# Optimization experiments

Hardware: AMD Instinct MI355X
Metric: run time of the kernel (lower is better)

The kernel has to match this reference:

```python
import jax, jax.numpy as jnp
import numpy as np

E4M3_MAX = 448.0  # max representable value of float8_e4m3fn


def _updated_scale(amax_history, amax_now, scale):
    # roll history, insert current amax, take running max (delayed scaling)
    hist = jnp.roll(amax_history, 1).at[0].set(amax_now)
    amax = jnp.max(hist)
    sf = E4M3_MAX / amax  # scale factor (margin = 0)
    sf = jnp.where((amax > 0.0) & jnp.isfinite(amax), sf, 1.0 / scale)
    return 1.0 / sf  # dequant scale


def _qdq(x, scale, amax_history):
    # quantize-dequantize through float8_e4m3fn with dynamic amax-history scaling
    amax_now = jnp.max(jnp.abs(x)).astype(jnp.float32)
    s = _updated_scale(amax_history, amax_now, scale[0])
    q = jnp.clip(x / s, -E4M3_MAX, E4M3_MAX).astype(jnp.float8_e4m3fn)
    return q.astype(x.dtype) * s


def setup_inputs() -> dict:
    key = jax.random.key(0)
    k1, k2 = jax.random.split(key, 2)
    B, S, D, F = 4, 2048, 4096, 16384
    HL = 16  # amax_history_length
    inputs = jax.random.normal(k1, (B, S, D), jnp.float32)
    # lecun_normal: std = 1/sqrt(fan_in)
    kernel = jax.random.normal(k2, (D, F), jnp.float32) * (1.0 / np.sqrt(D))
    bias = jnp.zeros((F,), jnp.float32)
    return {
        "inputs": inputs,
        "kernel": kernel,
        "bias": bias,
        "input_scale": jnp.ones((1,), jnp.float32),
        "input_amax_history": jnp.zeros((HL,), jnp.float32),
        "kernel_scale": jnp.ones((1,), jnp.float32),
        "kernel_amax_history": jnp.zeros((HL,), jnp.float32),
        "output_grad_scale": jnp.ones((1,), jnp.float32),
        "output_grad_amax_history": jnp.zeros((HL,), jnp.float32),
    }


def reference(inputs, kernel, bias, input_scale, input_amax_history,
              kernel_scale, kernel_amax_history, output_grad_scale,
              output_grad_amax_history):
    B, S, D = inputs.shape
    x = inputs.reshape(-1, D)  # (B*S, D)
    q_x = _qdq(x, input_scale, input_amax_history)
    q_k = _qdq(kernel, kernel_scale, kernel_amax_history)
    out = q_x @ q_k  # (B*S, F)
    # bias is rounded fp32->bf16->fp32 per the module
    b = bias.astype(jnp.bfloat16).astype(jnp.float32)
    out = jax.nn.gelu(out + b)
    return out.reshape(B, S, -1)
```

## Files before the change

### kernel.cpp

```cpp
#include <hip/hip_runtime.h>
#include <hip/hip_bf16.h>

typedef __attribute__((ext_vector_type(4))) int i32x4;
typedef __attribute__((ext_vector_type(8))) int i32x8;
typedef __attribute__((ext_vector_type(16))) float f32x16;

#define E4M3_MAX 448.0f
#define AS1 __attribute__((address_space(1)))
#define AS3 __attribute__((address_space(3)))

__device__ __forceinline__ float clip448(float v) {
  return fminf(fmaxf(v, -E4M3_MAX), E4M3_MAX);
}

__device__ __forceinline__ void gld_lds16(const void* g, void* l) {
  __builtin_amdgcn_global_load_lds((const AS1 void*)g, (AS3 void*)l, 16, 0, 0);
}

__device__ __forceinline__ float gelu_f(float v) {
  float y = 0.7978845608028654f * (v + 0.044715f * v * v * v);
  float a = fabsf(y);
  float z = __expf(-2.f * a);
  float th = (1.f - z) / (1.f + z);
  th = copysignf(th, y);
  return 0.5f * v * (1.f + th);
}

__global__ void init_ws_kernel(unsigned int* amax) {
  amax[0] = 0u;
  amax[1] = 0u;
}

__global__ void amax_kernel(const float* __restrict__ x, long n4,
                            unsigned int* __restrict__ amax_out) {
  long i0 = (long)blockIdx.x * blockDim.x + threadIdx.x;
  long stride = (long)gridDim.x * blockDim.x;
  const float4* x4 = (const float4*)x;
  float m = 0.f;
  for (long i = i0; i < n4; i += stride) {
    float4 v = x4[i];
    m = fmaxf(m, fmaxf(fmaxf(fabsf(v.x), fabsf(v.y)), fmaxf(fabsf(v.z), fabsf(v.w))));
  }
#pragma unroll
  for (int off = 32; off >= 1; off >>= 1)
    m = fmaxf(m, __shfl_xor(m, off));
  __shared__ float wmax[8];
  int wid = threadIdx.x >> 6;
  if ((threadIdx.x & 63) == 0) wmax[wid] = m;
  __syncthreads();
  if (threadIdx.x == 0) {
    int nw = blockDim.x >> 6;
    float bm = wmax[0];
    for (int w = 1; w < nw; ++w) bm = fmaxf(bm, wmax[w]);
    atomicMax(amax_out, __float_as_uint(bm));
  }
}

__global__ void scale_kernel(const unsigned int* __restrict__ amax,
                             const float* __restrict__ scale_x,
                             const float* __restrict__ hist_x,
                             const float* __restrict__ scale_k,
                             const float* __restrict__ hist_k,
                             int hl, float* __restrict__ scales) {
  if (threadIdx.x != 0) return;
  float ax = __uint_as_float(amax[0]);
  for (int i = 0; i < hl - 1; ++i) ax = fmaxf(ax, hist_x[i]);
  float sfx = E4M3_MAX / ax;
  if (!(ax > 0.f && isfinite(ax))) sfx = 1.f / scale_x[0];
  float sx = 1.f / sfx;
  float ak = __uint_as_float(amax[1]);
  for (int i = 0; i < hl - 1; ++i) ak = fmaxf(ak, hist_k[i]);
  float sfk = E4M3_MAX / ak;
  if (!(ak > 0.f && isfinite(ak))) sfk = 1.f / scale_k[0];
  float sk = 1.f / sfk;
  scales[0] = sx;
  scales[1] = sk;
  scales[2] = sx * sk;
}


__global__ void quant_x_kernel(const float* __restrict__ x,
                               unsigned char* __restrict__ Aq,
                               const float* __restrict__ scales, int K) {
  const float s = scales[0];
  const int kt = blockIdx.x, mt = blockIdx.y, nkt = gridDim.x;
  __shared__ float lt[128][68];
  const int t = threadIdx.x;
  const float* src = x + (size_t)mt * 128 * K + (size_t)kt * 64;
#pragma unroll
  for (int it = 0; it < 8; ++it) {
    int row = it * 16 + (t >> 4);
    int c4 = (t & 15) * 4;
    float4 v = *(const float4*)&src[(size_t)row * K + c4];
    lt[row][c4 + 0] = v.x; lt[row][c4 + 1] = v.y;
    lt[row][c4 + 2] = v.z; lt[row][c4 + 3] = v.w;
  }
  __syncthreads();
  uint4* out = (uint4*)(Aq + ((size_t)mt * nkt + kt) * 8192);
#pragma unroll
  for (int cc = 0; cc < 2; ++cc) {
    int c = t * 2 + cc;
    int g = c >> 7, h = (c >> 6) & 1, l = c & 63;
    int row = g * 32 + (l & 31);
    int kb = (l >> 5) * 32 + h * 16;
    unsigned int w[4];
#pragma unroll
    for (int q = 0; q < 4; ++q) {
      int b = kb + q * 4;
      int p = 0;
      p = __builtin_amdgcn_cvt_pk_fp8_f32(clip448(lt[row][b+0] / s), clip448(lt[row][b+1] / s), p, false);
      p = __builtin_amdgcn_cvt_pk_fp8_f32(clip448(lt[row][b+2] / s), clip448(lt[row][b+3] / s), p, true);
      w[q] = (unsigned int)p;
    }
    out[c] = make_uint4(w[0], w[1], w[2], w[3]);
  }
}

__global__ void quant_k_kernel(const float* __restrict__ w,
                               unsigned char* __restrict__ Bq,
                               const float* __restrict__ scales, int N) {
  const float s = scales[1];
  const int kt = blockIdx.x, nt = blockIdx.y, nkt = gridDim.x;
  __shared__ float lt[64][132];
  const int t = threadIdx.x;
  const float* src = w + (size_t)kt * 64 * N + (size_t)nt * 128;
#pragma unroll
  for (int it = 0; it < 8; ++it) {
    int row = it * 8 + (t >> 5);
    int c4 = (t & 31) * 4;
    float4 v = *(const float4*)&src[(size_t)row * N + c4];
    lt[row][c4 + 0] = v.x; lt[row][c4 + 1] = v.y;
    lt[row][c4 + 2] = v.z; lt[row][c4 + 3] = v.w;
  }
  __syncthreads();
  uint4* out = (uint4*)(Bq + ((size_t)nt * nkt + kt) * 8192);
#pragma unroll
  for (int cc = 0; cc < 2; ++cc) {
    int c = t * 2 + cc;
    int g = c >> 7, h = (c >> 6) & 1, l = c & 63;
    int nl = g * 32 + (l & 31);
    int kb = (l >> 5) * 32 + h * 16;
    unsigned int w4[4];
#pragma unroll
    for (int q = 0; q < 4; ++q) {
      int b = kb + q * 4;
      int p = 0;
      p = __builtin_amdgcn_cvt_pk_fp8_f32(clip448(lt[b+0][nl] / s), clip448(lt[b+1][nl] / s), p, false);
      p = __builtin_amdgcn_cvt_pk_fp8_f32(clip448(lt[b+2][nl] / s), clip448(lt[b+3][nl] / s), p, true);
      w4[q] = (unsigned int)p;
    }
    out[c] = make_uint4(w4[0], w4[1], w4[2], w4[3]);
  }
}

__global__ __launch_bounds__(512, 2) void gemm_fp8_kernel(
    const unsigned char* __restrict__ Aq, const unsigned char* __restrict__ Bq,
    const float* __restrict__ bias, const float* __restrict__ scales,
    float* __restrict__ C, int M, int N, int K) {
  __shared__ __align__(16) unsigned char lds[65536];
  const float s_xk = scales[2];
  const int nkt = K >> 6;
  const int t = threadIdx.x;
  const int lane = t & 63;
  const int wid = t >> 6;
  const int wm = wid >> 2, wn = wid & 3;

  int f = blockIdx.y * gridDim.x + blockIdx.x;
  int cpx = (gridDim.x * gridDim.y) >> 3;
  int f2 = (f & 7) * cpx + (f >> 3);
  int bx = f2 % gridDim.x;
  int by = f2 / gridDim.x;

  const size_t strideT = (size_t)nkt * 8192;
  const unsigned char* gA = Aq + (size_t)(2 * by) * strideT + t * 16;
  const unsigned char* gB = Bq + (size_t)(2 * bx) * strideT + t * 16;

  f32x16 acc[4][2];
#pragma unroll
  for (int i = 0; i < 4; ++i)
#pragma unroll
    for (int j = 0; j < 2; ++j)
#pragma unroll
      for (int r = 0; r < 16; ++r) acc[i][j][r] = 0.f;

  auto stage = [&](int buf, int kt_) {
    size_t o = (size_t)kt_ * 8192;
    unsigned char* l = lds + buf * 32768 + wid * 1024;
    gld_lds16(gA + o,           l);
    gld_lds16(gA + strideT + o, l + 8192);
    gld_lds16(gB + o,           l + 16384);
    gld_lds16(gB + strideT + o, l + 24576);
  };

  auto compute = [&](int buf) {
    const unsigned char* la = lds + buf * 32768;
    const unsigned char* lb = la + 16384;
    i32x8 av[4], bv[2];
#pragma unroll
    for (int i = 0; i < 4; ++i) {
      int g = wm * 4 + i;
      i32x4 lo = *(const i32x4*)&la[g * 2048 + lane * 16];
      i32x4 hi = *(const i32x4*)&la[g * 2048 + 1024 + lane * 16];
      av[i] = __builtin_shufflevector(lo, hi, 0, 1, 2, 3, 4, 5, 6, 7);
    }
#pragma unroll
    for (int j = 0; j < 2; ++j) {
      int g = wn * 2 + j;
      i32x4 lo = *(const i32x4*)&lb[g * 2048 + lane * 16];
      i32x4 hi = *(const i32x4*)&lb[g * 2048 + 1024 + lane * 16];
      bv[j] = __builtin_shufflevector(lo, hi, 0, 1, 2, 3, 4, 5, 6, 7);
    }
    __builtin_amdgcn_s_setprio(1);
#pragma unroll
    for (int i = 0; i < 4; ++i)
#pragma unroll
      for (int j = 0; j < 2; ++j)
        acc[i][j] = __builtin_amdgcn_mfma_scale_f32_32x32x64_f8f6f4(
            av[i], bv[j], acc[i][j], 0, 0, 0, 127, 0, 127);
    __builtin_amdgcn_s_setprio(0);
  };

  stage(0, 0);
  int buf = 0;
  for (int kt = 0; kt < nkt - 1; ++kt) {
    stage(buf ^ 1, kt + 1);
    asm volatile("s_waitcnt vmcnt(4)" ::: "memory");
    __builtin_amdgcn_s_barrier();
    asm volatile("" ::: "memory");
    compute(buf);
    asm volatile("" ::: "memory");
    __builtin_amdgcn_s_barrier();
    buf ^= 1;
  }
  asm volatile("s_waitcnt vmcnt(0)" ::: "memory");
  __builtin_amdgcn_s_barrier();
  asm volatile("" ::: "memory");
  compute(buf);

  const int m0 = by * 256;
  const int n0 = bx * 256;
  float bb[2];
#pragma unroll
  for (int j = 0; j < 2; ++j) {
    int col = n0 + wn * 64 + j * 32 + (lane & 31);
    bb[j] = __bfloat162float(__float2bfloat16(bias[col]));
  }
#pragma unroll
  for (int i = 0; i < 4; ++i) {
    int rowbase = m0 + wm * 128 + i * 32 + 4 * (lane >> 5);
#pragma unroll
    for (int j = 0; j < 2; ++j) {
      int col = n0 + wn * 64 + j * 32 + (lane & 31);
#pragma unroll
      for (int r = 0; r < 16; ++r) {
        int row = rowbase + (r & 3) + 8 * (r >> 2);
        float v = acc[i][j][r] * s_xk + bb[j];
        C[(size_t)row * N + col] = gelu_f(v);
      }
    }
  }
}

extern "C" void kernel_launch(void* const* d_in, const int* in_sizes, int n_in,
                              void* d_out, int out_size, void* d_ws, size_t ws_size,
                              hipStream_t stream) {
  const float* inputs = (const float*)d_in[0];
  const float* kernelw = (const float*)d_in[1];
  const float* bias = (const float*)d_in[2];
  const float* input_scale = (const float*)d_in[3];
  const float* input_hist = (const float*)d_in[4];
  const float* kernel_scale = (const float*)d_in[5];
  const float* kernel_hist = (const float*)d_in[6];

  const int F = in_sizes[2];
  const int D = in_sizes[1] / F;
  const long M = (long)in_sizes[0] / D;
  const int HL = in_sizes[4];
  const int N = F, K = D;

  unsigned int* amax = (unsigned int*)d_ws;
  float* scales = (float*)((char*)d_ws + 16);
  unsigned char* Aq = (unsigned char*)d_ws + 64;
  unsigned char* Bq = Aq + (size_t)M * K;

  float* C = (float*)d_out;

  init_ws_kernel<<<1, 1, 0, stream>>>(amax);
  amax_kernel<<<2048, 256, 0, stream>>>(inputs, (long)M * K / 4, &amax[0]);
  amax_kernel<<<2048, 256, 0, stream>>>(kernelw, (long)K * N / 4, &amax[1]);
  scale_kernel<<<1, 64, 0, stream>>>(amax, input_scale, input_hist, kernel_scale,
                                     kernel_hist, HL, scales);
  quant_x_kernel<<<dim3(K / 64, M / 128), 256, 0, stream>>>(inputs, Aq, scales, K);
  quant_k_kernel<<<dim3(K / 64, N / 128), 256, 0, stream>>>(kernelw, Bq, scales, N);
  gemm_fp8_kernel<<<dim3(N / 256, M / 256), 512, 0, stream>>>(Aq, Bq, bias, scales, C,
                                                              (int)M, N, K);
}
```

Before: 779.0 us.

## Shrink GEMM tile to 256x128 with register double-buffered fragments

Halves the N extent of each GEMM block tile from 256 to 128. LDS use drops to 48KB and each block now stages three 16-byte loads per k-step instead of four. The main loop is unrolled by two and prefetches the next k-step's LDS fragments into a second register set while the current MFMAs run. Output stores become nontemporal. Each block now does half the MFMAs per k-step, which lowers arithmetic intensity and doubles the grid and the total A-tile traffic, in exchange for more overlap and lower register and LDS pressure.

```diff
diff --git a/kernel.cpp b/kernel.cpp
--- a/kernel.cpp
+++ b/kernel.cpp
@@ -153,11 +153,41 @@
   }
 }
 
+#define BUFSZ 24576
+
+#define RD_FRAGS(av, bv, bufbase)                                              \
+  {                                                                            \
+    const unsigned char* la_ = lds + (bufbase);                                \
+    _Pragma("unroll") for (int i_ = 0; i_ < 4; ++i_) {                         \
+      int g_ = wm * 4 + i_;                                                    \
+      const unsigned char* p_ =                                                \
+          la_ + (g_ >> 2) * 8192 + (g_ & 3) * 2048 + lane * 16;                \
+      i32x4 lo_ = *(const i32x4*)p_;                                           \
+      i32x4 hi_ = *(const i32x4*)(p_ + 1024);                                  \
+      av[i_] = __builtin_shufflevector(lo_, hi_, 0, 1, 2, 3, 4, 5, 6, 7);      \
+    }                                                                          \
+    {                                                                          \
+      const unsigned char* p_ = la_ + 16384 + wn * 2048 + lane * 16;           \
+      i32x4 lo_ = *(const i32x4*)p_;                                           \
+      i32x4 hi_ = *(const i32x4*)(p_ + 1024);                                  \
+      bv = __builtin_shufflevector(lo_, hi_, 0, 1, 2, 3, 4, 5, 6, 7);          \
+    }                                                                          \
+  }
+
+#define MFMA_ALL(av, bv)                                                       \
+  {                                                                            \
+    __builtin_amdgcn_s_setprio(1);                                             \
+    _Pragma("unroll") for (int i_ = 0; i_ < 4; ++i_)                           \
+        acc[i_] = __builtin_amdgcn_mfma_scale_f32_32x32x64_f8f6f4(             \
+            av[i_], bv, acc[i_], 0, 0, 0, 127, 0, 127);                        \
+    __builtin_amdgcn_s_setprio(0);                                             \
+  }
+
 __global__ __launch_bounds__(512, 2) void gemm_fp8_kernel(
     const unsigned char* __restrict__ Aq, const unsigned char* __restrict__ Bq,
     const float* __restrict__ bias, const float* __restrict__ scales,
     float* __restrict__ C, int M, int N, int K) {
-  __shared__ __align__(16) unsigned char lds[65536];
+  __shared__ __align__(16) unsigned char lds[2 * BUFSZ];
   const float s_xk = scales[2];
   const int nkt = K >> 6;
   const int t = threadIdx.x;
@@ -173,90 +203,70 @@
 
   const size_t strideT = (size_t)nkt * 8192;
   const unsigned char* gA = Aq + (size_t)(2 * by) * strideT + t * 16;
-  const unsigned char* gB = Bq + (size_t)(2 * bx) * strideT + t * 16;
-
-  f32x16 acc[4][2];
+  const unsigned char* gB = Bq + (size_t)bx * strideT + t * 16;
+
+  f32x16 acc[4];
 #pragma unroll
   for (int i = 0; i < 4; ++i)
 #pragma unroll
-    for (int j = 0; j < 2; ++j)
-#pragma unroll
-      for (int r = 0; r < 16; ++r) acc[i][j][r] = 0.f;
-
-  auto stage = [&](int buf, int kt_) {
+    for (int r = 0; r < 16; ++r) acc[i][r] = 0.f;
+
+  auto stage = [&](unsigned bufbase, int kt_) {
     size_t o = (size_t)kt_ * 8192;
-    unsigned char* l = lds + buf * 32768 + wid * 1024;
+    unsigned char* l = lds + bufbase + wid * 1024;
     gld_lds16(gA + o,           l);
     gld_lds16(gA + strideT + o, l + 8192);
     gld_lds16(gB + o,           l + 16384);
-    gld_lds16(gB + strideT + o, l + 24576);
   };
 
-  auto compute = [&](int buf) {
-    const unsigned char* la = lds + buf * 32768;
-    const unsigned char* lb = la + 16384;
-    i32x8 av[4], bv[2];
-#pragma unroll
-    for (int i = 0; i < 4; ++i) {
-      int g = wm * 4 + i;
-      i32x4 lo = *(const i32x4*)&la[g * 2048 + lane * 16];
-      i32x4 hi = *(const i32x4*)&la[g * 2048 + 1024 + lane * 16];
-      av[i] = __builtin_shufflevector(lo, hi, 0, 1, 2, 3, 4, 5, 6, 7);
-    }
-#pragma unroll
-    for (int j = 0; j < 2; ++j) {
-      int g = wn * 2 + j;
-      i32x4 lo = *(const i32x4*)&lb[g * 2048 + lane * 16];
-      i32x4 hi = *(const i32x4*)&lb[g * 2048 + 1024 + lane * 16];
-      bv[j] = __builtin_shufflevector(lo, hi, 0, 1, 2, 3, 4, 5, 6, 7);
-    }
-    __builtin_amdgcn_s_setprio(1);
-#pragma unroll
-    for (int i = 0; i < 4; ++i)
-#pragma unroll
-      for (int j = 0; j < 2; ++j)
-        acc[i][j] = __builtin_amdgcn_mfma_scale_f32_32x32x64_f8f6f4(
-            av[i], bv[j], acc[i][j], 0, 0, 0, 127, 0, 127);
-    __builtin_amdgcn_s_setprio(0);
-  };
+  i32x8 avA[4], avB[4];
+  i32x8 bvA, bvB;
 
   stage(0, 0);
-  int buf = 0;
-  for (int kt = 0; kt < nkt - 1; ++kt) {
-    stage(buf ^ 1, kt + 1);
-    asm volatile("s_waitcnt vmcnt(4)" ::: "memory");
+  stage(BUFSZ, 1);
+  asm volatile("s_waitcnt vmcnt(3)" ::: "memory");
+  __builtin_amdgcn_s_barrier();
+  RD_FRAGS(avA, bvA, 0);
+  asm volatile("s_waitcnt lgkmcnt(0)" ::: "memory");
+
+  for (int kt = 0; kt + 1 < nkt; kt += 2) {
     __builtin_amdgcn_s_barrier();
-    asm volatile("" ::: "memory");
-    compute(buf);
-    asm volatile("" ::: "memory");
+    if (kt + 2 < nkt) {
+      stage(0, kt + 2);
+      asm volatile("s_waitcnt vmcnt(3)" ::: "memory");
+    } else {
+      asm volatile("s_waitcnt vmcnt(0)" ::: "memory");
+    }
     __builtin_amdgcn_s_barrier();
-    buf ^= 1;
-  }
-  asm volatile("s_waitcnt vmcnt(0)" ::: "memory");
-  __builtin_amdgcn_s_barrier();
-  asm volatile("" ::: "memory");
-  compute(buf);
+    RD_FRAGS(avB, bvB, BUFSZ);
+    MFMA_ALL(avA, bvA);
+    asm volatile("s_waitcnt lgkmcnt(0)" ::: "memory");
+
+    __builtin_amdgcn_s_barrier();
+    if (kt + 3 < nkt) {
+      stage(BUFSZ, kt + 3);
+      asm volatile("s_waitcnt vmcnt(3)" ::: "memory");
+    } else {
+      asm volatile("s_waitcnt vmcnt(0)" ::: "memory");
+    }
+    __builtin_amdgcn_s_barrier();
+    if (kt + 2 < nkt) { RD_FRAGS(avA, bvA, 0); }
+    MFMA_ALL(avB, bvB);
+    asm volatile("s_waitcnt lgkmcnt(0)" ::: "memory");
+  }
 
   const int m0 = by * 256;
-  const int n0 = bx * 256;
-  float bb[2];
-#pragma unroll
-  for (int j = 0; j < 2; ++j) {
-    int col = n0 + wn * 64 + j * 32 + (lane & 31);
-    bb[j] = __bfloat162float(__float2bfloat16(bias[col]));
-  }
+  const int n0 = bx * 128;
+  const int col = n0 + wn * 32 + (lane & 31);
+  const float bb = __bfloat162float(__float2bfloat16(bias[col]));
 #pragma unroll
   for (int i = 0; i < 4; ++i) {
     int rowbase = m0 + wm * 128 + i * 32 + 4 * (lane >> 5);
 #pragma unroll
-    for (int j = 0; j < 2; ++j) {
-      int col = n0 + wn * 64 + j * 32 + (lane & 31);
-#pragma unroll
-      for (int r = 0; r < 16; ++r) {
-        int row = rowbase + (r & 3) + 8 * (r >> 2);
-        float v = acc[i][j][r] * s_xk + bb[j];
-        C[(size_t)row * N + col] = gelu_f(v);
-      }
+    for (int r = 0; r < 16; ++r) {
+      int row = rowbase + (r & 3) + 8 * (r >> 2);
+      float v = acc[i][r] * s_xk + bb;
+      __builtin_nontemporal_store(gelu_f(v), &C[(size_t)row * N + col]);
     }
   }
 }
@@ -292,6 +302,6 @@
                                      kernel_hist, HL, scales);
   quant_x_kernel<<<dim3(K / 64, M / 128), 256, 0, stream>>>(inputs, Aq, scales, K);
   quant_k_kernel<<<dim3(K / 64, N / 128), 256, 0, stream>>>(kernelw, Bq, scales, N);
-  gemm_fp8_kernel<<<dim3(N / 256, M / 256), 512, 0, stream>>>(Aq, Bq, bias, scales, C,
+  gemm_fp8_kernel<<<dim3(N / 128, M / 256), 512, 0, stream>>>(Aq, Bq, bias, scales, C,
                                                               (int)M, N, K);
 }
```

Result: slower. 974.1 us (+25.0%).

## Triple-buffer LDS and interleave staged loads with split MFMA phases

Applied to the files above, without the earlier changes.

Moves the FP8 GEMM main loop from double to triple buffering, with prefetch two k-tiles ahead. Each iteration is split into two MFMA half-phases that interleave the A and B global-to-LDS loads, so memory latency is hidden behind compute. LDS use grows from 64KB to 96KB per block, which may hurt the two-blocks-per-CU occupancy target, and extra barriers are added. Output stores become nontemporal to reduce cache pollution from the large fp32 result.

```diff
diff --git a/kernel.cpp b/kernel.cpp
--- a/kernel.cpp
+++ b/kernel.cpp
@@ -153,11 +153,33 @@
   }
 }
 
+#define BUFSZ 32768
+
+#define RD_AV(dst, g_)                                                         \
+  {                                                                            \
+    const unsigned char* p_ =                                                  \
+        lds + cb + ((g_) >> 2) * 8192 + ((g_) & 3) * 2048 + lane * 16;         \
+    i32x4 lo_ = *(const i32x4*)p_;                                             \
+    i32x4 hi_ = *(const i32x4*)(p_ + 1024);                                    \
+    dst = __builtin_shufflevector(lo_, hi_, 0, 1, 2, 3, 4, 5, 6, 7);           \
+  }
+#define RD_BV(dst, g_)                                                         \
+  {                                                                            \
+    const unsigned char* p_ =                                                  \
+        lds + cb + 16384 + ((g_) >> 2) * 8192 + ((g_) & 3) * 2048 + lane * 16; \
+    i32x4 lo_ = *(const i32x4*)p_;                                             \
+    i32x4 hi_ = *(const i32x4*)(p_ + 1024);                                    \
+    dst = __builtin_shufflevector(lo_, hi_, 0, 1, 2, 3, 4, 5, 6, 7);           \
+  }
+#define MFMA1(r_, c_, a_, b_)                                                  \
+  acc[r_][c_] = __builtin_amdgcn_mfma_scale_f32_32x32x64_f8f6f4(               \
+      a_, b_, acc[r_][c_], 0, 0, 0, 127, 0, 127);
+
 __global__ __launch_bounds__(512, 2) void gemm_fp8_kernel(
     const unsigned char* __restrict__ Aq, const unsigned char* __restrict__ Bq,
     const float* __restrict__ bias, const float* __restrict__ scales,
     float* __restrict__ C, int M, int N, int K) {
-  __shared__ __align__(16) unsigned char lds[65536];
+  __shared__ __align__(16) unsigned char lds[3 * BUFSZ];
   const float s_xk = scales[2];
   const int nkt = K >> 6;
   const int t = threadIdx.x;
@@ -183,59 +205,64 @@
 #pragma unroll
       for (int r = 0; r < 16; ++r) acc[i][j][r] = 0.f;
 
-  auto stage = [&](int buf, int kt_) {
+  auto stageA = [&](unsigned bufbase, int kt_) {
     size_t o = (size_t)kt_ * 8192;
-    unsigned char* l = lds + buf * 32768 + wid * 1024;
+    unsigned char* l = lds + bufbase + wid * 1024;
     gld_lds16(gA + o,           l);
     gld_lds16(gA + strideT + o, l + 8192);
-    gld_lds16(gB + o,           l + 16384);
-    gld_lds16(gB + strideT + o, l + 24576);
   };
-
-  auto compute = [&](int buf) {
-    const unsigned char* la = lds + buf * 32768;
-    const unsigned char* lb = la + 16384;
-    i32x8 av[4], bv[2];
-#pragma unroll
-    for (int i = 0; i < 4; ++i) {
-      int g = wm * 4 + i;
-      i32x4 lo = *(const i32x4*)&la[g * 2048 + lane * 16];
-      i32x4 hi = *(const i32x4*)&la[g * 2048 + 1024 + lane * 16];
-      av[i] = __builtin_shufflevector(lo, hi, 0, 1, 2, 3, 4, 5, 6, 7);
+  auto stageB = [&](unsigned bufbase, int kt_) {
+    size_t o = (size_t)kt_ * 8192;
+    unsigned char* l = lds + bufbase + 16384 + wid * 1024;
+    gld_lds16(gB + o,           l);
+    gld_lds16(gB + strideT + o, l + 8192);
+  };
+
+  i32x8 av0, av1, av2, av3, bv0, bv1;
+
+  stageA(0, 0); stageB(0, 0);
+  stageA(BUFSZ, 1); stageB(BUFSZ, 1);
+  asm volatile("s_waitcnt vmcnt(4)" ::: "memory");
+  __builtin_amdgcn_s_barrier();
+
+  unsigned cb = 0;
+  for (int kt = 0; kt < nkt; ++kt) {
+    unsigned sb = cb + 2 * BUFSZ;
+    if (sb >= 3 * BUFSZ) sb -= 3 * BUFSZ;
+    const bool st = (kt + 2 < nkt);
+
+    RD_AV(av0, wm * 4 + 0);
+    RD_AV(av1, wm * 4 + 1);
+    RD_BV(bv0, wn * 2 + 0);
+    RD_BV(bv1, wn * 2 + 1);
+    if (st) stageA(sb, kt + 2);
+    __builtin_amdgcn_s_barrier();
+    asm volatile("s_waitcnt lgkmcnt(0)" ::: "memory");
+    __builtin_amdgcn_s_setprio(1);
+    MFMA1(0, 0, av0, bv0); MFMA1(0, 1, av0, bv1);
+    MFMA1(1, 0, av1, bv0); MFMA1(1, 1, av1, bv1);
+    __builtin_amdgcn_s_setprio(0);
+    __builtin_amdgcn_s_barrier();
+
+    RD_AV(av2, wm * 4 + 2);
+    RD_AV(av3, wm * 4 + 3);
+    if (st) {
+      stageB(sb, kt + 2);
+      asm volatile("s_waitcnt vmcnt(4)" ::: "memory");
+    } else if (kt + 1 < nkt) {
+      asm volatile("s_waitcnt vmcnt(0)" ::: "memory");
     }
-#pragma unroll
-    for (int j = 0; j < 2; ++j) {
-      int g = wn * 2 + j;
-      i32x4 lo = *(const i32x4*)&lb[g * 2048 + lane * 16];
-      i32x4 hi = *(const i32x4*)&lb[g * 2048 + 1024 + lane * 16];
-      bv[j] = __builtin_shufflevector(lo, hi, 0, 1, 2, 3, 4, 5, 6, 7);
-    }
+    __builtin_amdgcn_s_barrier();
+    asm volatile("s_waitcnt lgkmcnt(0)" ::: "memory");
     __builtin_amdgcn_s_setprio(1);
-#pragma unroll
-    for (int i = 0; i < 4; ++i)
-#pragma unroll
-      for (int j = 0; j < 2; ++j)
-        acc[i][j] = __builtin_amdgcn_mfma_scale_f32_32x32x64_f8f6f4(
-            av[i], bv[j], acc[i][j], 0, 0, 0, 127, 0, 127);
+    MFMA1(2, 0, av2, bv0); MFMA1(2, 1, av2, bv1);
+    MFMA1(3, 0, av3, bv0); MFMA1(3, 1, av3, bv1);
     __builtin_amdgcn_s_setprio(0);
-  };
-
-  stage(0, 0);
-  int buf = 0;
-  for (int kt = 0; kt < nkt - 1; ++kt) {
-    stage(buf ^ 1, kt + 1);
-    asm volatile("s_waitcnt vmcnt(4)" ::: "memory");
     __builtin_amdgcn_s_barrier();
-    asm volatile("" ::: "memory");
-    compute(buf);
-    asm volatile("" ::: "memory");
-    __builtin_amdgcn_s_barrier();
-    buf ^= 1;
-  }
-  asm volatile("s_waitcnt vmcnt(0)" ::: "memory");
-  __builtin_amdgcn_s_barrier();
-  asm volatile("" ::: "memory");
-  compute(buf);
+
+    cb += BUFSZ;
+    if (cb == 3 * BUFSZ) cb = 0;
+  }
 
   const int m0 = by * 256;
   const int n0 = bx * 256;
@@ -255,7 +282,7 @@
       for (int r = 0; r < 16; ++r) {
         int row = rowbase + (r & 3) + 8 * (r >> 2);
         float v = acc[i][j][r] * s_xk + bb[j];
-        C[(size_t)row * N + col] = gelu_f(v);
+        __builtin_nontemporal_store(gelu_f(v), &C[(size_t)row * N + col]);
       }
     }
   }
```

After: 756.5 us. 2.9% less time.
